# Performance work log

Measured on AMD Instinct MI355X. Metric: run time of the kernel, lower is better.

The kernel has to match this reference:

```python
import jax, jax.numpy as jnp
import numpy as np

BN_EPS = 1e-5
# regular 3x3 kernel grid offsets: row0 = dy, row1 = dx, kernel positions in row-major order
REG = jnp.array([[-1, -1, -1, 0, 0, 0, 1, 1, 1],
                 [-1,  0,  1, -1, 0, 1, -1, 0, 1]], dtype=jnp.float32)


def conv3x3(x, w, b):
    y = jax.lax.conv_general_dilated(x, w, window_strides=(1, 1),
                                     padding=((1, 1), (1, 1)),
                                     dimension_numbers=('NCHW', 'OIHW', 'NCHW'))
    return y + b[None, :, None, None]


def deform_conv3x3(x, dy, dx, w):
    # x: [N,C,H,W]; dy,dx: [N,9,H,W] per-kernel-tap offsets; w: [O,C,3,3]
    N, C, H, W = x.shape
    K = 9
    ky = jnp.repeat(jnp.arange(3), 3)   # [0,0,0,1,1,1,2,2,2]
    kx = jnp.tile(jnp.arange(3), 3)     # [0,1,2,0,1,2,0,1,2]
    # sampling positions: p = p_out - pad + k*dilation + offset (stride=1, pad=dil=1)
    py = dy + (jnp.arange(H) - 1)[None, None, :, None] + ky[None, :, None, None].astype(x.dtype)
    px = dx + (jnp.arange(W) - 1)[None, None, None, :] + kx[None, :, None, None].astype(x.dtype)
    y0 = jnp.floor(py)
    x0 = jnp.floor(px)
    wy = py - y0  # bilinear weights
    wx = px - x0
    y0i = y0.astype(jnp.int32)
    x0i = x0.astype(jnp.int32)
    nidx = jnp.arange(N)[:, None, None, None]

    def gather(yi, xi):
        valid = ((yi >= 0) & (yi < H) & (xi >= 0) & (xi < W)).astype(x.dtype)
        v = x[nidx, :, jnp.clip(yi, 0, H - 1), jnp.clip(xi, 0, W - 1)]  # [N,K,H,W,C]
        return v * valid[..., None]

    sampled = (gather(y0i,     x0i)     * ((1 - wy) * (1 - wx))[..., None]
             + gather(y0i,     x0i + 1) * ((1 - wy) * wx)[..., None]
             + gather(y0i + 1, x0i)     * (wy * (1 - wx))[..., None]
             + gather(y0i + 1, x0i + 1) * (wy * wx)[..., None])  # [N,K,H,W,C]
    O = w.shape[0]
    return jnp.einsum('nkhwc,ock->nohw', sampled, w.reshape(O, C, K))


def setup_inputs() -> dict:
    key = jax.random.key(0)
    ks = jax.random.split(key, 12)
    N, C, H, W = 2, 256, 96, 96
    O = 256
    sc = 1.0 / np.sqrt(C * 9)
    return {
        'x': jax.random.normal(ks[0], (N, C, H, W), jnp.float32),
        'mask_attention': jax.random.normal(ks[1], (N, C, H, W), jnp.float32),
        'w_tm': jax.random.normal(ks[2], (4, C, 3, 3), jnp.float32) * sc,
        'b_tm': jax.random.normal(ks[3], (4,), jnp.float32) * 0.01,
        'w_tr': jax.random.normal(ks[4], (2, C, 3, 3), jnp.float32) * sc,
        'b_tr': jax.random.normal(ks[5], (2,), jnp.float32) * 0.01,
        'w_deform': jax.random.normal(ks[6], (O, C, 3, 3), jnp.float32) * sc,
        'bn_gamma': jnp.ones((O,), jnp.float32),
        'bn_beta': jnp.zeros((O,), jnp.float32),
        'bn_mean': jax.random.normal(ks[7], (O,), jnp.float32) * 0.01,
        'bn_var': jax.random.uniform(ks[8], (O,), jnp.float32, 0.5, 1.5),
    }


def reference(x, mask_attention, w_tm, b_tm, w_tr, b_tr, w_deform,
              bn_gamma, bn_beta, bn_mean, bn_var):
    # mask_attention is overwritten by x in the original forward; ignored.
    N, C, H, W = x.shape
    tm = conv3x3(x, w_tm, b_tm)                       # [N,4,H,W]
    T = tm.transpose(0, 2, 3, 1).reshape(N, H, W, 2, 2)
    off = jnp.einsum('nhwij,jk->nhwik', T, REG) - REG  # [N,H,W,2,9], (T-I)@REG
    tr = conv3x3(x, w_tr, b_tr)                        # [N,2,H,W]
    off = off + tr.transpose(0, 2, 3, 1)[..., None]    # broadcast translation to all 9 taps
    dy = off[..., 0, :].transpose(0, 3, 1, 2)          # [N,9,H,W]
    dx = off[..., 1, :].transpose(0, 3, 1, 2)
    out = deform_conv3x3(x, dy, dx, w_deform)          # [N,O,H,W]
    inv = jax.lax.rsqrt(bn_var + BN_EPS)
    out = (out - bn_mean[None, :, None, None]) * (inv * bn_gamma)[None, :, None, None] \
          + bn_beta[None, :, None, None]
    return jax.nn.relu(out + x)
```

## Files before the change

### kernel.cpp

```cpp
#include <hip/hip_runtime.h>
#include <stdint.h>

#define H_ 96
#define W_ 96
#define C_ 256
#define O_ 256
#define N_ 2
#define HW_ (H_*W_)
#define M_ (N_*HW_)
#define GK 2304

typedef _Float16 f16x8 __attribute__((ext_vector_type(8)));
typedef _Float16 f16x2 __attribute__((ext_vector_type(2)));
typedef float f32x4 __attribute__((ext_vector_type(4)));
typedef unsigned short us4 __attribute__((ext_vector_type(4)));
typedef unsigned short us8 __attribute__((ext_vector_type(8)));

__device__ __forceinline__ unsigned short f2h(float f) {
  union { _Float16 h; unsigned short u; } v;
  v.h = (_Float16)f;
  return v.u;
}

__global__ __launch_bounds__(256) void k_pre(const float* __restrict__ x,
                                             const float* __restrict__ w_df,
                                             const float* __restrict__ w_tm,
                                             const float* __restrict__ w_tr,
                                             unsigned short* __restrict__ xt,
                                             unsigned short* __restrict__ wfrag,
                                             unsigned short* __restrict__ w6p) {
  const int b = blockIdx.x;
  const int tid = threadIdx.x;
  if (b < 576) {
    __shared__ unsigned short tile[64][130];
    const int pt = b % 144;
    const int ch = (b / 144) & 1;
    const int n  = b / 288;
    const int p0 = pt * 64, c0 = ch * 128;
    const float* xp = x + (size_t)n * C_ * HW_;
    unsigned short* xtp = xt + (size_t)n * C_ * HW_;
    const int tx = tid & 15, ty = tid >> 4;
#pragma unroll
    for (int pass = 0; pass < 8; pass++) {
      const int c = pass * 16 + ty;
      const f32x4 v = *(const f32x4*)(xp + (size_t)(c0 + c) * HW_ + p0 + tx * 4);
#pragma unroll
      for (int i = 0; i < 4; i++) tile[tx * 4 + i][c] = f2h(v[i]);
    }
    __syncthreads();
    const int l32 = tid & 31, pr = tid >> 5;
#pragma unroll
    for (int pass = 0; pass < 8; pass++) {
      const int p = pass * 8 + pr;
      us4 v;
#pragma unroll
      for (int i = 0; i < 4; i++) v[i] = tile[p][l32 * 4 + i];
      *(us4*)(xtp + (size_t)(p0 + p) * C_ + c0 + l32 * 4) = v;
    }
  } else if (b < 864) {
    const int base = (b - 576) * 2048 + tid * 8;
    const int l  = (base >> 3) & 63;
    const int g  = (base >> 9) & 15;
    const int ks = (base >> 13) & 7;
    const int t  = base >> 16;
    const int o  = g * 16 + (l & 15);
    const int c  = ks * 32 + (l >> 4) * 8;
    us8 res;
#pragma unroll
    for (int j = 0; j < 8; j++) res[j] = f2h(w_df[(size_t)(o * 256 + c + j) * 9 + t]);
    *(us8*)(wfrag + base) = res;
  } else {
    int idx = (b - 864) * 256 + tid;
    int t = idx >> 12;
    int r = idx & 4095;
    int j = r >> 8;
    int c = r & 255;
    float v = 0.f;
    if (j < 4) v = w_tm[(size_t)(j * C_ + c) * 9 + t];
    else if (j < 6) v = w_tr[(size_t)((j - 4) * C_ + c) * 9 + t];
    w6p[idx] = f2h(v);
  }
}

__global__ __launch_bounds__(512, 3) void k_fused(const unsigned short* __restrict__ xt,
                                                  const unsigned short* __restrict__ Wfrag,
                                                  const unsigned short* __restrict__ w6p,
                                                  const float* __restrict__ b_tm,
                                                  const float* __restrict__ b_tr,
                                                  const float* __restrict__ xres,
                                                  const float* __restrict__ gamma,
                                                  const float* __restrict__ beta,
                                                  const float* __restrict__ mean,
                                                  const float* __restrict__ var,
                                                  float* __restrict__ out) {
  __shared__ unsigned short As[2][32 * 256] __attribute__((aligned(16)));
  __shared__ float sred[8][16][8];
  __shared__ float coords_s[32][9][2];
  const int tid = threadIdx.x;
  const int wave = tid >> 6, lane = tid & 63;
  const int row = lane & 15, quad = lane >> 4;
  const int bm = (blockIdx.x & 7) * 72 + (blockIdx.x >> 3);
  const int m0 = bm * 32;
  const int n = m0 / HW_;
  const int sr = tid >> 4;
  const int cg = tid & 15;

  {
    const int hw0 = m0 - n * HW_;
    const int h = hw0 / W_;
    const int w0 = hw0 - h * W_;
    const int rh = wave >> 2;
    const int cq = (wave & 3) * 64;
    f32x4 oacc = {0.f, 0.f, 0.f, 0.f};
    const f16x8 zero8 = {};
#pragma unroll
    for (int t = 0; t < 9; t++) {
      const int ty = t / 3, tx = t % 3;
      const int y = h + ty - 1;
      if (y < 0 || y >= H_) continue;
      const int xx = w0 + rh * 16 + row + tx - 1;
      const bool valid = (xx >= 0) && (xx < W_);
      const int xc = min(max(xx, 0), W_ - 1);
      const unsigned short* arow =
          xt + (size_t)((n * H_ + y) * W_ + xc) * C_ + cq + quad * 8;
      const unsigned short* brow =
          w6p + (size_t)(t * 16 + row) * C_ + cq + quad * 8;
#pragma unroll
      for (int ks = 0; ks < 2; ks++) {
        f16x8 av = *(const f16x8*)(const void*)(arow + ks * 32);
        if (!valid) av = zero8;
        f16x8 bv = *(const f16x8*)(const void*)(brow + ks * 32);
        oacc = __builtin_amdgcn_mfma_f32_16x16x32_f16(av, bv, oacc, 0, 0, 0);
      }
    }
    if (row < 6) {
#pragma unroll
      for (int r = 0; r < 4; r++) sred[wave][quad * 4 + r][row] = oacc[r];
    }
  }
  __syncthreads();
  if (wave < 2 && lane < 16) {
    const int rg = wave * 16 + lane;
    const int hwm = m0 + rg - n * HW_;
    const int h = hwm / W_, w = hwm - h * W_;
    float a[6];
#pragma unroll
    for (int j = 0; j < 6; j++)
      a[j] = sred[wave * 4 + 0][lane][j] + sred[wave * 4 + 1][lane][j] +
             sred[wave * 4 + 2][lane][j] + sred[wave * 4 + 3][lane][j];
    const float tm0 = a[0] + b_tm[0];
    const float tm1 = a[1] + b_tm[1];
    const float tm2 = a[2] + b_tm[2];
    const float tm3 = a[3] + b_tm[3];
    const float tr0 = a[4] + b_tr[0];
    const float tr1 = a[5] + b_tr[1];
#pragma unroll
    for (int t = 0; t < 9; t++) {
      const float ry = (float)(t / 3) - 1.f;
      const float rx = (float)(t % 3) - 1.f;
      coords_s[rg][t][0] = (float)h + tr0 + tm0 * ry + tm1 * rx;
      coords_s[rg][t][1] = (float)w + tr1 + tm2 * ry + tm3 * rx;
    }
  }
  __syncthreads();

  f32x4 acc0[2] = {}, acc1[2] = {};
  f16x2 cwh0, cwh1, cwh2, cwh3;
  int cb[4];
  us8 u0[4], u1[4];

#define PREP1(TAP)                                                             \
  {                                                                            \
    const float py = coords_s[sr][TAP][0];                                     \
    const float px = coords_s[sr][TAP][1];                                     \
    const float fy = floorf(py), fx = floorf(px);                              \
    const float wy = py - fy, wx = px - fx;                                    \
    const int y0 = (int)fy, x0 = (int)fx;                                      \
    const int y1 = y0 + 1, x1 = x0 + 1;                                        \
    const float vy0 = (y0 >= 0 && y0 < H_) ? 1.f : 0.f;                        \
    const float vy1 = (y1 >= 0 && y1 < H_) ? 1.f : 0.f;                        \
    const float vx0 = (x0 >= 0 && x0 < W_) ? 1.f : 0.f;                        \
    const float vx1 = (x1 >= 0 && x1 < W_) ? 1.f : 0.f;                        \
    const float c0f = (1.f - wy) * (1.f - wx) * vy0 * vx0;                     \
    const float c1f = (1.f - wy) * wx * vy0 * vx1;                             \
    const float c2f = wy * (1.f - wx) * vy1 * vx0;                             \
    const float c3f = wy * wx * vy1 * vx1;                                     \
    const _Float16 h0 = (_Float16)c0f, h1 = (_Float16)c1f;                     \
    const _Float16 h2 = (_Float16)c2f, h3 = (_Float16)c3f;                     \
    cwh0 = (f16x2){h0, h0}; cwh1 = (f16x2){h1, h1};                            \
    cwh2 = (f16x2){h2, h2}; cwh3 = (f16x2){h3, h3};                            \
    const int cy0 = min(max(y0, 0), H_ - 1), cy1 = min(max(y1, 0), H_ - 1);    \
    const int cx0 = min(max(x0, 0), W_ - 1), cx1 = min(max(x1, 0), W_ - 1);    \
    cb[0] = ((n * H_ + cy0) * W_ + cx0) * C_;                                  \
    cb[1] = ((n * H_ + cy0) * W_ + cx1) * C_;                                  \
    cb[2] = ((n * H_ + cy1) * W_ + cx0) * C_;                                  \
    cb[3] = ((n * H_ + cy1) * W_ + cx1) * C_;                                  \
  }

#define LOADC1()                                                               \
  {                                                                            \
    const int cc = cg * 16;                                                    \
    u0[0] = *(const us8*)(xt + cb[0] + cc); u1[0] = *(const us8*)(xt + cb[0] + cc + 8); \
    u0[1] = *(const us8*)(xt + cb[1] + cc); u1[1] = *(const us8*)(xt + cb[1] + cc + 8); \
    u0[2] = *(const us8*)(xt + cb[2] + cc); u1[2] = *(const us8*)(xt + cb[2] + cc + 8); \
    u0[3] = *(const us8*)(xt + cb[3] + cc); u1[3] = *(const us8*)(xt + cb[3] + cc + 8); \
  }

#define LERP8V(DST, U)                                                         \
  {                                                                            \
    const f16x2* p0 = (const f16x2*)&U[0];                                     \
    const f16x2* p1 = (const f16x2*)&U[1];                                     \
    const f16x2* p2 = (const f16x2*)&U[2];                                     \
    const f16x2* p3 = (const f16x2*)&U[3];                                     \
    f16x2* d = (f16x2*)&DST;                                                   \
    _Pragma("unroll")                                                          \
    for (int p = 0; p < 4; p++) {                                              \
      f16x2 r = p0[p] * cwh0;                                                  \
      r = p1[p] * cwh1 + r;                                                    \
      r = p2[p] * cwh2 + r;                                                    \
      r = p3[p] * cwh3 + r;                                                    \
      d[p] = r;                                                                \
    }                                                                          \
  }

  PREP1(0);
  LOADC1();

  for (int tap = 0; tap < 9; tap++) {
    unsigned short* __restrict__ asb = As[tap & 1];

    const unsigned short* wfTap =
        Wfrag + (size_t)(tap * 8) * 8192 + wave * 1024 + lane * 8;
    f16x8 bv[2];
#pragma unroll
    for (int ot = 0; ot < 2; ot++) bv[ot] = *(const f16x8*)(const void*)(wfTap + ot * 512);

    {
      const int q0 = cg * 2, q1 = cg * 2 + 1;
      const int s0 = (q0 & 24) | ((q0 ^ sr) & 7);
      const int s1 = (q1 & 24) | ((q1 ^ sr) & 7);
      us8 r0, r1;
      LERP8V(r0, u0);
      LERP8V(r1, u1);
      *(us8*)(void*)&asb[sr * 256 + s0 * 8] = r0;
      *(us8*)(void*)&asb[sr * 256 + s1 * 8] = r1;
    }

    __syncthreads();

    if (tap < 8) {
      PREP1(tap + 1);
      LOADC1();
    }

#pragma unroll
    for (int ks = 0; ks < 8; ks++) {
      const int q = ks * 4 + quad;
      const int slot = (q & 24) | ((q ^ row) & 7);
      const f16x8 av0 = *(const f16x8*)(const void*)&asb[row * 256 + slot * 8];
      const f16x8 av1 = *(const f16x8*)(const void*)&asb[(row + 16) * 256 + slot * 8];
      f16x8 bn[2];
      if (ks < 7) {
        const unsigned short* wfn = wfTap + (size_t)(ks + 1) * 8192;
#pragma unroll
        for (int ot = 0; ot < 2; ot++) bn[ot] = *(const f16x8*)(const void*)(wfn + ot * 512);
      }
#pragma unroll
      for (int ot = 0; ot < 2; ot++)
        acc0[ot] = __builtin_amdgcn_mfma_f32_16x16x32_f16(av0, bv[ot], acc0[ot], 0, 0, 0);
#pragma unroll
      for (int ot = 0; ot < 2; ot++)
        acc1[ot] = __builtin_amdgcn_mfma_f32_16x16x32_f16(av1, bv[ot], acc1[ot], 0, 0, 0);
      if (ks < 7) {
#pragma unroll
        for (int ot = 0; ot < 2; ot++) bv[ot] = bn[ot];
      }
    }
  }

  const int hwb = m0 - n * HW_ + quad * 4;
#pragma unroll
  for (int ot = 0; ot < 2; ot++) {
    const int o = wave * 32 + ot * 16 + row;
    const float sc = rsqrtf(var[o] + 1e-5f) * gamma[o];
    const float bi = beta[o] - mean[o] * sc;
    const size_t ob0 = (size_t)(n * O_ + o) * HW_ + hwb;
    f32x4 rv = *(const f32x4*)(xres + ob0);
    f32x4 ov;
#pragma unroll
    for (int r = 0; r < 4; r++) ov[r] = fmaxf(acc0[ot][r] * sc + bi + rv[r], 0.f);
    *(f32x4*)(out + ob0) = ov;
    const size_t ob1 = ob0 + 16;
    rv = *(const f32x4*)(xres + ob1);
#pragma unroll
    for (int r = 0; r < 4; r++) ov[r] = fmaxf(acc1[ot][r] * sc + bi + rv[r], 0.f);
    *(f32x4*)(out + ob1) = ov;
  }
}

extern "C" void kernel_launch(void* const* d_in, const int* in_sizes, int n_in,
                              void* d_out, int out_size, void* d_ws, size_t ws_size,
                              hipStream_t stream) {
  const float* x     = (const float*)d_in[0];
  const float* w_tm  = (const float*)d_in[2];
  const float* b_tm  = (const float*)d_in[3];
  const float* w_tr  = (const float*)d_in[4];
  const float* b_tr  = (const float*)d_in[5];
  const float* w_df  = (const float*)d_in[6];
  const float* gamma = (const float*)d_in[7];
  const float* beta  = (const float*)d_in[8];
  const float* mean  = (const float*)d_in[9];
  const float* var   = (const float*)d_in[10];
  float* out = (float*)d_out;

  char* ws = (char*)d_ws;
  unsigned short* xt    = (unsigned short*)(ws);
  unsigned short* wfrag = (unsigned short*)(ws + 9437184);
  unsigned short* w6p   = (unsigned short*)(ws + 9437184 + 1179648);

  k_pre<<<1008, 256, 0, stream>>>(x, w_df, w_tm, w_tr, xt, wfrag, w6p);
  k_fused<<<576, 512, 0, stream>>>(xt, wfrag, w6p, b_tm, b_tr, x,
                                   gamma, beta, mean, var, out);
}
```

Measured before the change: 184.2 us.

## Process both batch images per block to reuse weight fragments

Each block now handles the same 32 spatial positions for both batch samples, so every loaded weight fragment feeds twice as many MFMAs. The grid is halved to 288 blocks and launch bounds drop to 2 blocks per SM. The software prefetch of the next tap's gather is removed and the gather, lerp and store now happen inline before the barrier. This cuts global weight traffic, but it exposes gather latency, raises register and LDS pressure, and leaves fewer blocks than CUs (288 against the MI355X's 256 CUs), which risks poor load balance.

Result: no change. 184.5 us (+0.1%).

```diff
diff --git a/kernel.cpp b/kernel.cpp
--- a/kernel.cpp
+++ b/kernel.cpp
@@ -20,6 +20,10 @@
   union { _Float16 h; unsigned short u; } v;
   v.h = (_Float16)f;
   return v.u;
+}
+__device__ __forceinline__ f16x2 hpair(float f) {
+  const _Float16 h = (_Float16)f;
+  return (f16x2){h, h};
 }
 
 __global__ __launch_bounds__(256) void k_pre(const float* __restrict__ x,
@@ -82,7 +86,7 @@
   }
 }
 
-__global__ __launch_bounds__(512, 3) void k_fused(const unsigned short* __restrict__ xt,
+__global__ __launch_bounds__(512, 2) void k_fused(const unsigned short* __restrict__ xt,
                                                   const unsigned short* __restrict__ Wfrag,
                                                   const unsigned short* __restrict__ w6p,
                                                   const float* __restrict__ b_tm,
@@ -93,86 +97,85 @@
                                                   const float* __restrict__ mean,
                                                   const float* __restrict__ var,
                                                   float* __restrict__ out) {
-  __shared__ unsigned short As[2][32 * 256] __attribute__((aligned(16)));
+  __shared__ unsigned short As[2][2][32 * 256] __attribute__((aligned(16)));
   __shared__ float sred[8][16][8];
-  __shared__ float coords_s[32][9][2];
+  __shared__ float coords_s[2][32][9][2];
   const int tid = threadIdx.x;
   const int wave = tid >> 6, lane = tid & 63;
   const int row = lane & 15, quad = lane >> 4;
-  const int bm = (blockIdx.x & 7) * 72 + (blockIdx.x >> 3);
+  const int bm = (blockIdx.x & 7) * 36 + (blockIdx.x >> 3);
   const int m0 = bm * 32;
-  const int n = m0 / HW_;
   const int sr = tid >> 4;
   const int cg = tid & 15;
 
-  {
-    const int hw0 = m0 - n * HW_;
-    const int h = hw0 / W_;
-    const int w0 = hw0 - h * W_;
-    const int rh = wave >> 2;
-    const int cq = (wave & 3) * 64;
-    f32x4 oacc = {0.f, 0.f, 0.f, 0.f};
-    const f16x8 zero8 = {};
-#pragma unroll
-    for (int t = 0; t < 9; t++) {
-      const int ty = t / 3, tx = t % 3;
-      const int y = h + ty - 1;
-      if (y < 0 || y >= H_) continue;
-      const int xx = w0 + rh * 16 + row + tx - 1;
-      const bool valid = (xx >= 0) && (xx < W_);
-      const int xc = min(max(xx, 0), W_ - 1);
-      const unsigned short* arow =
-          xt + (size_t)((n * H_ + y) * W_ + xc) * C_ + cq + quad * 8;
-      const unsigned short* brow =
-          w6p + (size_t)(t * 16 + row) * C_ + cq + quad * 8;
-#pragma unroll
-      for (int ks = 0; ks < 2; ks++) {
-        f16x8 av = *(const f16x8*)(const void*)(arow + ks * 32);
-        if (!valid) av = zero8;
-        f16x8 bv = *(const f16x8*)(const void*)(brow + ks * 32);
-        oacc = __builtin_amdgcn_mfma_f32_16x16x32_f16(av, bv, oacc, 0, 0, 0);
-      }
-    }
-    if (row < 6) {
-#pragma unroll
-      for (int r = 0; r < 4; r++) sred[wave][quad * 4 + r][row] = oacc[r];
-    }
-  }
-  __syncthreads();
-  if (wave < 2 && lane < 16) {
-    const int rg = wave * 16 + lane;
-    const int hwm = m0 + rg - n * HW_;
-    const int h = hwm / W_, w = hwm - h * W_;
-    float a[6];
-#pragma unroll
-    for (int j = 0; j < 6; j++)
-      a[j] = sred[wave * 4 + 0][lane][j] + sred[wave * 4 + 1][lane][j] +
-             sred[wave * 4 + 2][lane][j] + sred[wave * 4 + 3][lane][j];
-    const float tm0 = a[0] + b_tm[0];
-    const float tm1 = a[1] + b_tm[1];
-    const float tm2 = a[2] + b_tm[2];
-    const float tm3 = a[3] + b_tm[3];
-    const float tr0 = a[4] + b_tr[0];
-    const float tr1 = a[5] + b_tr[1];
-#pragma unroll
-    for (int t = 0; t < 9; t++) {
-      const float ry = (float)(t / 3) - 1.f;
-      const float rx = (float)(t % 3) - 1.f;
-      coords_s[rg][t][0] = (float)h + tr0 + tm0 * ry + tm1 * rx;
-      coords_s[rg][t][1] = (float)w + tr1 + tm2 * ry + tm3 * rx;
-    }
-  }
-  __syncthreads();
-
-  f32x4 acc0[2] = {}, acc1[2] = {};
+  for (int s = 0; s < 2; ++s) {
+    const unsigned short* xts = xt + (size_t)s * C_ * HW_;
+    {
+      const int h = m0 / W_;
+      const int w0 = m0 - h * W_;
+      const int rh = wave >> 2;
+      const int cq = (wave & 3) * 64;
+      f32x4 oacc = {0.f, 0.f, 0.f, 0.f};
+      const f16x8 zero8 = {};
+#pragma unroll
+      for (int t = 0; t < 9; t++) {
+        const int ty = t / 3, tx = t % 3;
+        const int y = h + ty - 1;
+        if (y < 0 || y >= H_) continue;
+        const int xx = w0 + rh * 16 + row + tx - 1;
+        const bool valid = (xx >= 0) && (xx < W_);
+        const int xc = min(max(xx, 0), W_ - 1);
+        const unsigned short* arow = xts + (size_t)(y * W_ + xc) * C_ + cq + quad * 8;
+        const unsigned short* brow = w6p + (size_t)(t * 16 + row) * C_ + cq + quad * 8;
+#pragma unroll
+        for (int ks = 0; ks < 2; ks++) {
+          f16x8 av = *(const f16x8*)(const void*)(arow + ks * 32);
+          if (!valid) av = zero8;
+          f16x8 bv = *(const f16x8*)(const void*)(brow + ks * 32);
+          oacc = __builtin_amdgcn_mfma_f32_16x16x32_f16(av, bv, oacc, 0, 0, 0);
+        }
+      }
+      if (row < 6) {
+#pragma unroll
+        for (int r = 0; r < 4; r++) sred[wave][quad * 4 + r][row] = oacc[r];
+      }
+    }
+    __syncthreads();
+    if (wave < 2 && lane < 16) {
+      const int rg = wave * 16 + lane;
+      const int hwm = m0 + rg;
+      const int h = hwm / W_, w = hwm - h * W_;
+      float a[6];
+#pragma unroll
+      for (int j = 0; j < 6; j++)
+        a[j] = sred[wave * 4 + 0][lane][j] + sred[wave * 4 + 1][lane][j] +
+               sred[wave * 4 + 2][lane][j] + sred[wave * 4 + 3][lane][j];
+      const float tm0 = a[0] + b_tm[0];
+      const float tm1 = a[1] + b_tm[1];
+      const float tm2 = a[2] + b_tm[2];
+      const float tm3 = a[3] + b_tm[3];
+      const float tr0 = a[4] + b_tr[0];
+      const float tr1 = a[5] + b_tr[1];
+#pragma unroll
+      for (int t = 0; t < 9; t++) {
+        const float ry = (float)(t / 3) - 1.f;
+        const float rx = (float)(t % 3) - 1.f;
+        coords_s[s][rg][t][0] = (float)h + tr0 + tm0 * ry + tm1 * rx;
+        coords_s[s][rg][t][1] = (float)w + tr1 + tm2 * ry + tm3 * rx;
+      }
+    }
+    __syncthreads();
+  }
+
+  f32x4 acc[2][2][2] = {};
   f16x2 cwh0, cwh1, cwh2, cwh3;
   int cb[4];
   us8 u0[4], u1[4];
 
-#define PREP1(TAP)                                                             \
+#define PREP1(TAP, S)                                                          \
   {                                                                            \
-    const float py = coords_s[sr][TAP][0];                                     \
-    const float px = coords_s[sr][TAP][1];                                     \
+    const float py = coords_s[S][sr][TAP][0];                                  \
+    const float px = coords_s[S][sr][TAP][1];                                  \
     const float fy = floorf(py), fx = floorf(px);                              \
     const float wy = py - fy, wx = px - fx;                                    \
     const int y0 = (int)fy, x0 = (int)fx;                                      \
@@ -181,29 +184,25 @@
     const float vy1 = (y1 >= 0 && y1 < H_) ? 1.f : 0.f;                        \
     const float vx0 = (x0 >= 0 && x0 < W_) ? 1.f : 0.f;                        \
     const float vx1 = (x1 >= 0 && x1 < W_) ? 1.f : 0.f;                        \
-    const float c0f = (1.f - wy) * (1.f - wx) * vy0 * vx0;                     \
-    const float c1f = (1.f - wy) * wx * vy0 * vx1;                             \
-    const float c2f = wy * (1.f - wx) * vy1 * vx0;                             \
-    const float c3f = wy * wx * vy1 * vx1;                                     \
-    const _Float16 h0 = (_Float16)c0f, h1 = (_Float16)c1f;                     \
-    const _Float16 h2 = (_Float16)c2f, h3 = (_Float16)c3f;                     \
-    cwh0 = (f16x2){h0, h0}; cwh1 = (f16x2){h1, h1};                            \
-    cwh2 = (f16x2){h2, h2}; cwh3 = (f16x2){h3, h3};                            \
+    cwh0 = hpair((1.f - wy) * (1.f - wx) * vy0 * vx0);                         \
+    cwh1 = hpair((1.f - wy) * wx * vy0 * vx1);                                 \
+    cwh2 = hpair(wy * (1.f - wx) * vy1 * vx0);                                 \
+    cwh3 = hpair(wy * wx * vy1 * vx1);                                         \
     const int cy0 = min(max(y0, 0), H_ - 1), cy1 = min(max(y1, 0), H_ - 1);    \
     const int cx0 = min(max(x0, 0), W_ - 1), cx1 = min(max(x1, 0), W_ - 1);    \
-    cb[0] = ((n * H_ + cy0) * W_ + cx0) * C_;                                  \
-    cb[1] = ((n * H_ + cy0) * W_ + cx1) * C_;                                  \
-    cb[2] = ((n * H_ + cy1) * W_ + cx0) * C_;                                  \
-    cb[3] = ((n * H_ + cy1) * W_ + cx1) * C_;                                  \
-  }
-
-#define LOADC1()                                                               \
+    cb[0] = (cy0 * W_ + cx0) * C_;                                             \
+    cb[1] = (cy0 * W_ + cx1) * C_;                                             \
+    cb[2] = (cy1 * W_ + cx0) * C_;                                             \
+    cb[3] = (cy1 * W_ + cx1) * C_;                                             \
+  }
+
+#define LOADC1(XB)                                                             \
   {                                                                            \
     const int cc = cg * 16;                                                    \
-    u0[0] = *(const us8*)(xt + cb[0] + cc); u1[0] = *(const us8*)(xt + cb[0] + cc + 8); \
-    u0[1] = *(const us8*)(xt + cb[1] + cc); u1[1] = *(const us8*)(xt + cb[1] + cc + 8); \
-    u0[2] = *(const us8*)(xt + cb[2] + cc); u1[2] = *(const us8*)(xt + cb[2] + cc + 8); \
-    u0[3] = *(const us8*)(xt + cb[3] + cc); u1[3] = *(const us8*)(xt + cb[3] + cc + 8); \
+    u0[0] = *(const us8*)(XB + cb[0] + cc); u1[0] = *(const us8*)(XB + cb[0] + cc + 8); \
+    u0[1] = *(const us8*)(XB + cb[1] + cc); u1[1] = *(const us8*)(XB + cb[1] + cc + 8); \
+    u0[2] = *(const us8*)(XB + cb[2] + cc); u1[2] = *(const us8*)(XB + cb[2] + cc + 8); \
+    u0[3] = *(const us8*)(XB + cb[3] + cc); u1[3] = *(const us8*)(XB + cb[3] + cc + 8); \
   }
 
 #define LERP8V(DST, U)                                                         \
@@ -223,42 +222,46 @@
     }                                                                          \
   }
 
-  PREP1(0);
-  LOADC1();
+#define STAGE(TAP, S, XB)                                                      \
+  {                                                                            \
+    PREP1(TAP, S);                                                             \
+    LOADC1(XB);                                                                \
+    unsigned short* asb = &As[(TAP) & 1][S][0];                                \
+    const int q0i = cg * 2, q1i = cg * 2 + 1;                                  \
+    const int s0 = (q0i & 24) | ((q0i ^ sr) & 7);                              \
+    const int s1 = (q1i & 24) | ((q1i ^ sr) & 7);                              \
+    us8 r0, r1;                                                                \
+    LERP8V(r0, u0);                                                            \
+    LERP8V(r1, u1);                                                            \
+    *(us8*)(void*)&asb[sr * 256 + s0 * 8] = r0;                                \
+    *(us8*)(void*)&asb[sr * 256 + s1 * 8] = r1;                                \
+  }
+
+  const unsigned short* xt1 = xt + (size_t)C_ * HW_;
 
   for (int tap = 0; tap < 9; tap++) {
-    unsigned short* __restrict__ asb = As[tap & 1];
+    STAGE(tap, 0, xt);
+    STAGE(tap, 1, xt1);
 
     const unsigned short* wfTap =
-        Wfrag + (size_t)(tap * 8) * 8192 + wave * 1024 + lane * 8;
+        Wfrag + (size_t)tap * 65536 + wave * 1024 + lane * 8;
     f16x8 bv[2];
 #pragma unroll
     for (int ot = 0; ot < 2; ot++) bv[ot] = *(const f16x8*)(const void*)(wfTap + ot * 512);
-
-    {
-      const int q0 = cg * 2, q1 = cg * 2 + 1;
-      const int s0 = (q0 & 24) | ((q0 ^ sr) & 7);
-      const int s1 = (q1 & 24) | ((q1 ^ sr) & 7);
-      us8 r0, r1;
-      LERP8V(r0, u0);
-      LERP8V(r1, u1);
-      *(us8*)(void*)&asb[sr * 256 + s0 * 8] = r0;
-      *(us8*)(void*)&asb[sr * 256 + s1 * 8] = r1;
-    }
+    __builtin_amdgcn_sched_barrier(0);
 
     __syncthreads();
 
-    if (tap < 8) {
-      PREP1(tap + 1);
-      LOADC1();
-    }
-
+    const unsigned short* A0 = &As[tap & 1][0][0];
+    const unsigned short* A1 = &As[tap & 1][1][0];
 #pragma unroll
     for (int ks = 0; ks < 8; ks++) {
       const int q = ks * 4 + quad;
       const int slot = (q & 24) | ((q ^ row) & 7);
-      const f16x8 av0 = *(const f16x8*)(const void*)&asb[row * 256 + slot * 8];
-      const f16x8 av1 = *(const f16x8*)(const void*)&asb[(row + 16) * 256 + slot * 8];
+      const f16x8 a00 = *(const f16x8*)(const void*)&A0[row * 256 + slot * 8];
+      const f16x8 a01 = *(const f16x8*)(const void*)&A0[(row + 16) * 256 + slot * 8];
+      const f16x8 a10 = *(const f16x8*)(const void*)&A1[row * 256 + slot * 8];
+      const f16x8 a11 = *(const f16x8*)(const void*)&A1[(row + 16) * 256 + slot * 8];
       f16x8 bn[2];
       if (ks < 7) {
         const unsigned short* wfn = wfTap + (size_t)(ks + 1) * 8192;
@@ -266,11 +269,12 @@
         for (int ot = 0; ot < 2; ot++) bn[ot] = *(const f16x8*)(const void*)(wfn + ot * 512);
       }
 #pragma unroll
-      for (int ot = 0; ot < 2; ot++)
-        acc0[ot] = __builtin_amdgcn_mfma_f32_16x16x32_f16(av0, bv[ot], acc0[ot], 0, 0, 0);
-#pragma unroll
-      for (int ot = 0; ot < 2; ot++)
-        acc1[ot] = __builtin_amdgcn_mfma_f32_16x16x32_f16(av1, bv[ot], acc1[ot], 0, 0, 0);
+      for (int ot = 0; ot < 2; ot++) {
+        acc[0][0][ot] = __builtin_amdgcn_mfma_f32_16x16x32_f16(a00, bv[ot], acc[0][0][ot], 0, 0, 0);
+        acc[0][1][ot] = __builtin_amdgcn_mfma_f32_16x16x32_f16(a01, bv[ot], acc[0][1][ot], 0, 0, 0);
+        acc[1][0][ot] = __builtin_amdgcn_mfma_f32_16x16x32_f16(a10, bv[ot], acc[1][0][ot], 0, 0, 0);
+        acc[1][1][ot] = __builtin_amdgcn_mfma_f32_16x16x32_f16(a11, bv[ot], acc[1][1][ot], 0, 0, 0);
+      }
       if (ks < 7) {
 #pragma unroll
         for (int ot = 0; ot < 2; ot++) bv[ot] = bn[ot];
@@ -278,23 +282,26 @@
     }
   }
 
-  const int hwb = m0 - n * HW_ + quad * 4;
+  const int hwb = m0 + quad * 4;
 #pragma unroll
   for (int ot = 0; ot < 2; ot++) {
     const int o = wave * 32 + ot * 16 + row;
     const float sc = rsqrtf(var[o] + 1e-5f) * gamma[o];
     const float bi = beta[o] - mean[o] * sc;
-    const size_t ob0 = (size_t)(n * O_ + o) * HW_ + hwb;
-    f32x4 rv = *(const f32x4*)(xres + ob0);
-    f32x4 ov;
-#pragma unroll
-    for (int r = 0; r < 4; r++) ov[r] = fmaxf(acc0[ot][r] * sc + bi + rv[r], 0.f);
-    *(f32x4*)(out + ob0) = ov;
-    const size_t ob1 = ob0 + 16;
-    rv = *(const f32x4*)(xres + ob1);
-#pragma unroll
-    for (int r = 0; r < 4; r++) ov[r] = fmaxf(acc1[ot][r] * sc + bi + rv[r], 0.f);
-    *(f32x4*)(out + ob1) = ov;
+#pragma unroll
+    for (int s = 0; s < 2; ++s) {
+      const size_t ob0 = (size_t)(s * O_ + o) * HW_ + hwb;
+      f32x4 rv = *(const f32x4*)(xres + ob0);
+      f32x4 ov;
+#pragma unroll
+      for (int r = 0; r < 4; r++) ov[r] = fmaxf(acc[s][0][ot][r] * sc + bi + rv[r], 0.f);
+      *(f32x4*)(out + ob0) = ov;
+      const size_t ob1 = ob0 + 16;
+      rv = *(const f32x4*)(xres + ob1);
+#pragma unroll
+      for (int r = 0; r < 4; r++) ov[r] = fmaxf(acc[s][1][ot][r] * sc + bi + rv[r], 0.f);
+      *(f32x4*)(out + ob1) = ov;
+    }
   }
 }
 
@@ -319,6 +326,6 @@
   unsigned short* w6p   = (unsigned short*)(ws + 9437184 + 1179648);
 
   k_pre<<<1008, 256, 0, stream>>>(x, w_df, w_tm, w_tr, xt, wfrag, w6p);
-  k_fused<<<576, 512, 0, stream>>>(xt, wfrag, w6p, b_tm, b_tr, x,
+  k_fused<<<288, 512, 0, stream>>>(xt, wfrag, w6p, b_tm, b_tr, x,
                                    gamma, beta, mean, var, out);
 }
```
